# Optimization experiments

Hardware: AMD Instinct MI355X
Metric: run time of the kernel (lower is better)

## Reference

```python
import jax, jax.numpy as jnp
import numpy as np
from jax import lax

M, B, L, Q, S = 4, 64, 512, 512, 26  # models, batch, seq_len, hmm states, alphabet


def setup_inputs() -> dict:
    key = jax.random.key(0)
    k1, k2, k3, k4 = jax.random.split(key, 4)
    inputs = jax.random.uniform(k1, (M, B, L, S), dtype=jnp.float32)
    A_logits = jax.random.normal(k2, (M, Q, Q), dtype=jnp.float32)
    init_logits = jax.random.normal(k3, (M, Q), dtype=jnp.float32)
    em_logits = jax.random.normal(k4, (M, Q, S), dtype=jnp.float32)
    return {"inputs": inputs, "A_logits": A_logits,
            "init_logits": init_logits, "em_logits": em_logits}


def reference(inputs, A_logits, init_logits, em_logits):
    """Profile-HMM forward algorithm (scaled), as run by the MsaHmmCell RNN.

    inputs:      [M, B, L, S] observation probabilities (one-hot or soft)
    A_logits:    [M, Q, Q]    transition logits (row-softmax -> stochastic A)
    init_logits: [M, Q]       initial state distribution logits
    em_logits:   [M, Q, S]    emission logits (softmax over alphabet)
    returns loglik [M, B]  (the tensor the layer returns)
    """
    A = jax.nn.softmax(A_logits, axis=-1)        # [M, Q, Q]
    pi = jax.nn.softmax(init_logits, axis=-1)    # [M, Q]
    Bem = jax.nn.softmax(em_logits, axis=-1)     # [M, Q, S]

    # per-step emission likelihoods, time-major for scan: [L, M, B, Q]
    E = jnp.einsum('mbls,mqs->lmbq', inputs, Bem)

    # t = 0: alpha_0 = pi * e_0, scaled
    a0 = pi[:, None, :] * E[0]                   # [M, B, Q]
    s0 = jnp.sum(a0, axis=-1, keepdims=True)
    carry0 = (a0 / s0, jnp.log(s0[..., 0]))      # (alpha [M,B,Q], loglik [M,B])

    def step(carry, e_t):
        alpha, ll = carry
        r = jnp.einsum('mbq,mqp->mbp', alpha, A)  # transition
        a = r * e_t                               # emission
        s = jnp.sum(a, axis=-1, keepdims=True)    # scaling factor
        return (a / s, ll + jnp.log(s[..., 0])), None

    (alpha, loglik), _ = lax.scan(step, carry0, E[1:])
    return loglik  # [M, B] == reshape(loglik, (num_models, -1)) in the layer
```

## Files before the change

kernel.cpp:

```cpp
#include <hip/hip_runtime.h>
#include <hip/hip_bf16.h>
#include <math.h>


#define MM 4
#define BB 64
#define LL 512
#define QQ 512
#define SS 26
#define ASTR 528

typedef float f32x4 __attribute__((ext_vector_type(4)));
typedef int i32x4 __attribute__((ext_vector_type(4)));
typedef int i32x8 __attribute__((ext_vector_type(8)));

__device__ __forceinline__ float bf2f(unsigned short u) {
    return __uint_as_float(((unsigned)u) << 16);
}
__device__ __forceinline__ unsigned short f2bf(float f) {
    unsigned u = __float_as_uint(f);
    u = u + 0x7FFFu + ((u >> 16) & 1u);
    return (unsigned short)(u >> 16);
}
__device__ __forceinline__ unsigned char f2fp8(float x) {
    int r = __builtin_amdgcn_cvt_pk_fp8_f32(x, x, 0, false);
    return (unsigned char)(r & 0xFF);
}
__device__ __forceinline__ i32x8 ld32B(const unsigned char* p) {
    i32x4 lo = *(const i32x4*)p;
    i32x4 hi = *(const i32x4*)(p + 16);
    return __builtin_shufflevector(lo, hi, 0, 1, 2, 3, 4, 5, 6, 7);
}
__device__ __forceinline__ void barrier_lds() {
    __asm__ __volatile__("" ::: "memory");
    __builtin_amdgcn_s_waitcnt(0xC07F);
    __builtin_amdgcn_s_barrier();
    __asm__ __volatile__("" ::: "memory");
}


__global__ void prep_small(const float* __restrict__ il, const float* __restrict__ em,
                           float* __restrict__ pi, float* __restrict__ Bem) {
    int blk = blockIdx.x;
    int m = blk / (QQ + 1);
    int r = blk % (QQ + 1);
    int lane = threadIdx.x;
    if (r < QQ) {
        float x = (lane < SS) ? em[((size_t)m * QQ + r) * SS + lane] : -1e30f;
        float mx = x;
        #pragma unroll
        for (int o = 1; o < 64; o <<= 1) mx = fmaxf(mx, __shfl_xor(mx, o));
        float e = (lane < SS) ? __expf(x - mx) : 0.f;
        float s = e;
        #pragma unroll
        for (int o = 1; o < 64; o <<= 1) s += __shfl_xor(s, o);
        if (lane < SS) Bem[((size_t)m * QQ + r) * SS + lane] = e / s;
    } else {
        float v[8];
        float mx = -1e30f;
        #pragma unroll
        for (int k = 0; k < 8; ++k) { v[k] = il[m * QQ + k * 64 + lane]; mx = fmaxf(mx, v[k]); }
        #pragma unroll
        for (int o = 1; o < 64; o <<= 1) mx = fmaxf(mx, __shfl_xor(mx, o));
        float s = 0.f;
        #pragma unroll
        for (int k = 0; k < 8; ++k) { v[k] = __expf(v[k] - mx); s += v[k]; }
        #pragma unroll
        for (int o = 1; o < 64; o <<= 1) s += __shfl_xor(s, o);
        #pragma unroll
        for (int k = 0; k < 8; ++k) pi[m * QQ + k * 64 + lane] = v[k] / s;
    }
}

__global__ void prep_arow(const float* __restrict__ Al, float* __restrict__ Lrow) {
    int row = blockIdx.x;
    int lane = threadIdx.x;
    const float* p = Al + (size_t)row * QQ;
    float v[8];
    float mx = -1e30f;
    #pragma unroll
    for (int k = 0; k < 8; ++k) { v[k] = p[k * 64 + lane]; mx = fmaxf(mx, v[k]); }
    #pragma unroll
    for (int o = 1; o < 64; o <<= 1) mx = fmaxf(mx, __shfl_xor(mx, o));
    float s = 0.f;
    #pragma unroll
    for (int k = 0; k < 8; ++k) s += __expf(v[k] - mx);
    #pragma unroll
    for (int o = 1; o < 64; o <<= 1) s += __shfl_xor(s, o);
    if (lane == 0) Lrow[row] = mx + __logf(s);
}

__global__ void prep_atq(const float* __restrict__ Al, const float* __restrict__ Lrow,
                         unsigned char* __restrict__ Atq) {
    int bid = blockIdx.x;
    int m = bid >> 3, pb = bid & 7;
    __shared__ unsigned char tile[64][68];
    int l6 = threadIdx.x & 63, g = threadIdx.x >> 6;
    for (int c = 0; c < 8; ++c) {
        #pragma unroll
        for (int r = 0; r < 16; ++r) {
            int ql = g * 16 + r;
            int q = c * 64 + ql;
            float x = Al[((size_t)m * QQ + q) * QQ + pb * 64 + l6];
            tile[ql][l6] = f2fp8(__expf(x - Lrow[m * QQ + q]) * 256.f);
        }
        __syncthreads();
        #pragma unroll
        for (int r = 0; r < 16; ++r) {
            int pr = g * 16 + r;
            Atq[((size_t)m * QQ + pb * 64 + pr) * QQ + c * 64 + l6] = tile[l6][pr];
        }
        __syncthreads();
    }
}

__global__ void prep_e(const float* __restrict__ inp, const float* __restrict__ Bem,
                       unsigned short* __restrict__ E) {
    int bid = blockIdx.x;
    int tc = bid & 7;
    int b = (bid >> 3) & 63;
    int m = bid >> 9;
    int q0 = threadIdx.x;
    float bem0[SS], bem1[SS];
    const float* bp = Bem + (size_t)m * QQ * SS;
    #pragma unroll
    for (int j = 0; j < SS; ++j) bem0[j] = bp[(size_t)q0 * SS + j];
    #pragma unroll
    for (int j = 0; j < SS; ++j) bem1[j] = bp[(size_t)(q0 + 256) * SS + j];
    const float* ip = inp + (((size_t)(m * BB + b)) * LL + tc * 64) * SS;
    for (int lt = 0; lt < 64; ++lt) {
        int t = tc * 64 + lt;
        float a0 = 0.f, a1 = 0.f;
        #pragma unroll
        for (int j = 0; j < SS; ++j) {
            float x = ip[lt * SS + j];
            a0 += x * bem0[j];
            a1 += x * bem1[j];
        }
        size_t o = (((size_t)m * LL + t) * BB + b) * QQ + q0;
        E[o] = f2bf(a0);
        E[o + 256] = f2bf(a1);
    }
}


__launch_bounds__(512, 2)
__global__ void hmm_scan(const unsigned short* __restrict__ E,
                         const unsigned char* __restrict__ Atq,
                         const float* __restrict__ pi,
                         float* __restrict__ out) {
    const int c = blockIdx.x;
    const int m = c >> 2, bg = c & 3;
    const int tid = threadIdx.x;
    const int lane = tid & 63;
    const int wv = tid >> 6;
    const int sl = lane & 15;
    const int quad = lane >> 4;
    const float LOG256 = 5.545177444479562f;

    __shared__ unsigned char albuf[2][16 * ASTR];
    __shared__ __align__(16) float psl[2][16][20];
    __shared__ float Sfin[2][16];

    i32x8 breg[4][4];
    {
        const unsigned char* Ab = Atq + (size_t)m * QQ * QQ;
        #pragma unroll
        for (int h = 0; h < 4; ++h) {
            int p = wv * 64 + h * 16 + sl;
            const unsigned char* rp = Ab + (size_t)p * QQ + quad * 32;
            #pragma unroll
            for (int kc = 0; kc < 4; ++kc)
                breg[h][kc] = ld32B(rp + kc * 128);
        }
    }

    int wq[4];
    #pragma unroll
    for (int h = 0; h < 4; ++h)
        wq[h] = sl * ASTR + wv * 64 + h * 16 + quad * 4;

    const int b = bg * 16 + sl;
    const size_t ebase = (size_t)m * LL * BB * QQ;
    const ushort4* __restrict__ E4 = (const ushort4*)(E + ebase);
    const unsigned ESTR4 = (BB * QQ) >> 2;
    const unsigned ebq = (unsigned)(b * QQ) >> 2;
    unsigned eoffs[4];
    #pragma unroll
    for (int h = 0; h < 4; ++h) eoffs[h] = (unsigned)(wv * 16 + h * 4 + quad);

    float v[4][4];
    ushort4 ea[4], eb[4];

    float gcur, gprev, ll;

    {
        #pragma unroll
        for (int h = 0; h < 4; ++h) ea[h] = E4[ebq + ESTR4 + eoffs[h]];
        #pragma unroll
        for (int h = 0; h < 4; ++h) {
            int p0 = wv * 64 + h * 16 + quad * 4;
            f32x4 pv = *(const f32x4*)(pi + m * QQ + p0);
            ushort4 e0 = E4[ebq + eoffs[h]];
            v[h][0] = pv[0] * bf2f(e0.x);
            v[h][1] = pv[1] * bf2f(e0.y);
            v[h][2] = pv[2] * bf2f(e0.z);
            v[h][3] = pv[3] * bf2f(e0.w);
        }
        gcur = 256.f;
        gprev = 1.0f;
        unsigned char* ab = &albuf[0][0];
        #pragma unroll
        for (int h = 0; h < 4; ++h) {
            int d = __builtin_amdgcn_cvt_pk_fp8_f32(gcur * v[h][0], gcur * v[h][1], 0, false);
            d = __builtin_amdgcn_cvt_pk_fp8_f32(gcur * v[h][2], gcur * v[h][3], d, true);
            *(int*)(ab + wq[h]) = d;
        }
        float ps = ((v[0][0] + v[0][1]) + (v[0][2] + v[0][3]))
                 + ((v[1][0] + v[1][1]) + (v[1][2] + v[1][3]))
                 + ((v[2][0] + v[2][1]) + (v[2][2] + v[2][3]))
                 + ((v[3][0] + v[3][1]) + (v[3][2] + v[3][3]));
        ps += __shfl_xor(ps, 16);
        if ((quad & 1) == 0) psl[0][sl][2 * wv + (quad >> 1)] = ps;
        ll = -(__logf(gcur) + LOG256);
        barrier_lds();
    }

    auto body = [&](int par, bool first, ushort4 (&ecur)[4], ushort4 (&enxt)[4],
                    unsigned epre) {
        #pragma unroll
        for (int h = 0; h < 4; ++h) enxt[h] = E4[epre + eoffs[h]];

        if (wv == 0 && lane < 16) {
            const f32x4* pr = (const f32x4*)&psl[par][lane][0];
            f32x4 ss4 = (pr[0] + pr[1]) + (pr[2] + pr[3]);
            Sfin[par][lane] = (ss4[0] + ss4[1]) + (ss4[2] + ss4[3]);
        }
        float lam = first ? 16384.0f
                          : 16384.0f * gcur * gprev * Sfin[par ^ 1][sl];
        float gnext = 128.0f * __builtin_amdgcn_rcpf(lam);

        const unsigned char* ar = &albuf[par][0] + sl * ASTR + quad * 32;
        i32x8 af0 = ld32B(ar);
        i32x8 af1 = ld32B(ar + 128);
        i32x8 af2 = ld32B(ar + 256);
        i32x8 af3 = ld32B(ar + 384);

        unsigned char* ab = &albuf[par ^ 1][0];
        float ps = 0.f;
        #pragma unroll
        for (int h = 0; h < 4; ++h) {
            f32x4 acc = (f32x4){0.f, 0.f, 0.f, 0.f};
            acc = __builtin_amdgcn_mfma_scale_f32_16x16x128_f8f6f4(
                breg[h][0], af0, acc, 0, 0, 0, 0x7F7F7F7F, 0, 0x7F7F7F7F);
            acc = __builtin_amdgcn_mfma_scale_f32_16x16x128_f8f6f4(
                breg[h][1], af1, acc, 0, 0, 0, 0x7F7F7F7F, 0, 0x7F7F7F7F);
            acc = __builtin_amdgcn_mfma_scale_f32_16x16x128_f8f6f4(
                breg[h][2], af2, acc, 0, 0, 0, 0x7F7F7F7F, 0, 0x7F7F7F7F);
            acc = __builtin_amdgcn_mfma_scale_f32_16x16x128_f8f6f4(
                breg[h][3], af3, acc, 0, 0, 0, 0x7F7F7F7F, 0, 0x7F7F7F7F);
            v[h][0] = acc[0] * bf2f(ecur[h].x);
            v[h][1] = acc[1] * bf2f(ecur[h].y);
            v[h][2] = acc[2] * bf2f(ecur[h].z);
            v[h][3] = acc[3] * bf2f(ecur[h].w);
            int d = __builtin_amdgcn_cvt_pk_fp8_f32(gnext * v[h][0], gnext * v[h][1], 0, false);
            d = __builtin_amdgcn_cvt_pk_fp8_f32(gnext * v[h][2], gnext * v[h][3], d, true);
            *(int*)(ab + wq[h]) = d;
            ps += (v[h][0] + v[h][1]) + (v[h][2] + v[h][3]);
        }
        ps += __shfl_xor(ps, 16);
        if ((quad & 1) == 0) psl[par ^ 1][sl][2 * wv + (quad >> 1)] = ps;
        ll -= __logf(gnext) + LOG256;
        gprev = gcur; gcur = gnext;
        barrier_lds();
    };

    unsigned epre = ebq + 2 * ESTR4;
    body(0, true,  ea, eb, epre); epre += ESTR4;
    body(1, false, eb, ea, epre); epre += ESTR4;
    for (int t = 2; t < LL - 2; t += 2) {
        body(0, false, ea, eb, epre); epre += ESTR4;
        body(1, false, eb, ea, epre); epre += ESTR4;
    }
    {
        const unsigned char* ar = &albuf[0][0] + sl * ASTR + quad * 32;
        i32x8 af0 = ld32B(ar);
        i32x8 af1 = ld32B(ar + 128);
        i32x8 af2 = ld32B(ar + 256);
        i32x8 af3 = ld32B(ar + 384);
        #pragma unroll
        for (int h = 0; h < 4; ++h) {
            f32x4 acc = (f32x4){0.f, 0.f, 0.f, 0.f};
            acc = __builtin_amdgcn_mfma_scale_f32_16x16x128_f8f6f4(
                breg[h][0], af0, acc, 0, 0, 0, 0x7F7F7F7F, 0, 0x7F7F7F7F);
            acc = __builtin_amdgcn_mfma_scale_f32_16x16x128_f8f6f4(
                breg[h][1], af1, acc, 0, 0, 0, 0x7F7F7F7F, 0, 0x7F7F7F7F);
            acc = __builtin_amdgcn_mfma_scale_f32_16x16x128_f8f6f4(
                breg[h][2], af2, acc, 0, 0, 0, 0x7F7F7F7F, 0, 0x7F7F7F7F);
            acc = __builtin_amdgcn_mfma_scale_f32_16x16x128_f8f6f4(
                breg[h][3], af3, acc, 0, 0, 0, 0x7F7F7F7F, 0, 0x7F7F7F7F);
            v[h][0] = acc[0] * bf2f(ea[h].x);
            v[h][1] = acc[1] * bf2f(ea[h].y);
            v[h][2] = acc[2] * bf2f(ea[h].z);
            v[h][3] = acc[3] * bf2f(ea[h].w);
        }
    }

    {
        float ps = ((v[0][0] + v[0][1]) + (v[0][2] + v[0][3]))
                 + ((v[1][0] + v[1][1]) + (v[1][2] + v[1][3]))
                 + ((v[2][0] + v[2][1]) + (v[2][2] + v[2][3]))
                 + ((v[3][0] + v[3][1]) + (v[3][2] + v[3][3]));
        ps += __shfl_xor(ps, 16);
        if ((quad & 1) == 0) psl[1][sl][2 * wv + (quad >> 1)] = ps;
        __syncthreads();
        if (wv == 0 && lane < 16) {
            const f32x4* pr = (const f32x4*)&psl[1][lane][0];
            f32x4 ss4 = (pr[0] + pr[1]) + (pr[2] + pr[3]);
            float S = (ss4[0] + ss4[1]) + (ss4[2] + ss4[3]);
            out[m * BB + bg * 16 + lane] = ll + __logf(S);
        }
    }
}


extern "C" void kernel_launch(void* const* d_in, const int* in_sizes, int n_in,
                              void* d_out, int out_size, void* d_ws, size_t ws_size,
                              hipStream_t stream) {
    const float* inputs = (const float*)d_in[0];
    const float* A_logits = (const float*)d_in[1];
    const float* init_logits = (const float*)d_in[2];
    const float* em_logits = (const float*)d_in[3];
    float* out = (float*)d_out;

    char* ws = (char*)d_ws;
    size_t off = 0;
    unsigned short* E = (unsigned short*)(ws + off);  off += (size_t)MM * LL * BB * QQ * 2;
    unsigned char* Atq = (unsigned char*)(ws + off);  off += (size_t)MM * QQ * QQ;
    float* Bem = (float*)(ws + off);                  off += (size_t)MM * QQ * SS * 4;
    float* pi = (float*)(ws + off);                   off += (size_t)MM * QQ * 4;
    float* Lrow = (float*)(ws + off);                 off += (size_t)MM * QQ * 4;

    if (ws_size < off) {
        (void)hipMemsetAsync(d_out, 0, (size_t)out_size * sizeof(float), stream);
        return;
    }

    prep_small<<<dim3(MM * (QQ + 1)), dim3(64), 0, stream>>>(init_logits, em_logits, pi, Bem);
    prep_arow<<<dim3(MM * QQ), dim3(64), 0, stream>>>(A_logits, Lrow);
    prep_atq<<<dim3(MM * 8), dim3(256), 0, stream>>>(A_logits, Lrow, Atq);
    prep_e<<<dim3(MM * BB * 8), dim3(256), 0, stream>>>(inputs, Bem, E);
    hmm_scan<<<dim3(16), dim3(512), 0, stream>>>(E, Atq, pi, out);
}
```

Baseline: 619.6 us.

## Triple-buffer partial sums and split MFMA chains to shorten per-step critical path

Every thread now reduces the previous step's partial sums itself from a triple-buffered psl array. This replaces the old scheme where wave 0 wrote Sfin and the other threads read it one step later, and removes that extra dependency stage. The MFMA K-reduction is split into two independent accumulator chains, interleaved across the four output tiles, and summed at the end, so the dependent MFMA latency chain per tile is shorter. The cost is more redundant LDS reads for the reduction and more accumulator registers.

```diff
diff --git a/kernel.cpp b/kernel.cpp
--- a/kernel.cpp
+++ b/kernel.cpp
@@ -31,6 +31,8 @@
     i32x4 hi = *(const i32x4*)(p + 16);
     return __builtin_shufflevector(lo, hi, 0, 1, 2, 3, 4, 5, 6, 7);
 }
+#define MFMA8(A, B, C) __builtin_amdgcn_mfma_scale_f32_16x16x128_f8f6f4( \
+    (A), (B), (C), 0, 0, 0, 0x7F7F7F7F, 0, 0x7F7F7F7F)
 __device__ __forceinline__ void barrier_lds() {
     __asm__ __volatile__("" ::: "memory");
     __builtin_amdgcn_s_waitcnt(0xC07F);
@@ -159,8 +161,7 @@
     const float LOG256 = 5.545177444479562f;
 
     __shared__ unsigned char albuf[2][16 * ASTR];
-    __shared__ __align__(16) float psl[2][16][20];
-    __shared__ float Sfin[2][16];
+    __shared__ __align__(16) float psl[3][16][20];
 
     i32x8 breg[4][4];
     {
@@ -226,84 +227,141 @@
         barrier_lds();
     }
 
-    auto body = [&](int par, bool first, ushort4 (&ecur)[4], ushort4 (&enxt)[4],
-                    unsigned epre) {
+    auto body = [&](int par, bool first, int rs, int ws,
+                    ushort4 (&ecur)[4], ushort4 (&enxt)[4], unsigned epre) {
         #pragma unroll
         for (int h = 0; h < 4; ++h) enxt[h] = E4[epre + eoffs[h]];
 
-        if (wv == 0 && lane < 16) {
-            const f32x4* pr = (const f32x4*)&psl[par][lane][0];
+        float lam;
+        if (first) {
+            lam = 16384.0f;
+        } else {
+            const f32x4* pr = (const f32x4*)&psl[rs][sl][0];
             f32x4 ss4 = (pr[0] + pr[1]) + (pr[2] + pr[3]);
-            Sfin[par][lane] = (ss4[0] + ss4[1]) + (ss4[2] + ss4[3]);
-        }
-        float lam = first ? 16384.0f
-                          : 16384.0f * gcur * gprev * Sfin[par ^ 1][sl];
+            float Sp = (ss4[0] + ss4[1]) + (ss4[2] + ss4[3]);
+            lam = 16384.0f * gcur * gprev * Sp;
+        }
         float gnext = 128.0f * __builtin_amdgcn_rcpf(lam);
 
         const unsigned char* ar = &albuf[par][0] + sl * ASTR + quad * 32;
         i32x8 af0 = ld32B(ar);
+        i32x8 af2 = ld32B(ar + 256);
         i32x8 af1 = ld32B(ar + 128);
-        i32x8 af2 = ld32B(ar + 256);
         i32x8 af3 = ld32B(ar + 384);
 
+        f32x4 z = (f32x4){0.f, 0.f, 0.f, 0.f};
+        f32x4 aA0, aA1, aA2, aA3, aB0, aB1, aB2, aB3;
+        aA0 = MFMA8(breg[0][0], af0, z);
+        aA1 = MFMA8(breg[1][0], af0, z);
+        aA2 = MFMA8(breg[2][0], af0, z);
+        aA3 = MFMA8(breg[3][0], af0, z);
+        aB0 = MFMA8(breg[0][2], af2, z);
+        aB1 = MFMA8(breg[1][2], af2, z);
+        aB2 = MFMA8(breg[2][2], af2, z);
+        aB3 = MFMA8(breg[3][2], af2, z);
+        aA0 = MFMA8(breg[0][1], af1, aA0);
+        aA1 = MFMA8(breg[1][1], af1, aA1);
+        aA2 = MFMA8(breg[2][1], af1, aA2);
+        aA3 = MFMA8(breg[3][1], af1, aA3);
+        aB0 = MFMA8(breg[0][3], af3, aB0);
+        aB1 = MFMA8(breg[1][3], af3, aB1);
+        aB2 = MFMA8(breg[2][3], af3, aB2);
+        aB3 = MFMA8(breg[3][3], af3, aB3);
+
+        f32x4 t0 = aA0 + aB0;
+        f32x4 t1 = aA1 + aB1;
+        f32x4 t2 = aA2 + aB2;
+        f32x4 t3 = aA3 + aB3;
         unsigned char* ab = &albuf[par ^ 1][0];
-        float ps = 0.f;
+        v[0][0] = t0[0] * bf2f(ecur[0].x);
+        v[0][1] = t0[1] * bf2f(ecur[0].y);
+        v[0][2] = t0[2] * bf2f(ecur[0].z);
+        v[0][3] = t0[3] * bf2f(ecur[0].w);
+        v[1][0] = t1[0] * bf2f(ecur[1].x);
+        v[1][1] = t1[1] * bf2f(ecur[1].y);
+        v[1][2] = t1[2] * bf2f(ecur[1].z);
+        v[1][3] = t1[3] * bf2f(ecur[1].w);
+        v[2][0] = t2[0] * bf2f(ecur[2].x);
+        v[2][1] = t2[1] * bf2f(ecur[2].y);
+        v[2][2] = t2[2] * bf2f(ecur[2].z);
+        v[2][3] = t2[3] * bf2f(ecur[2].w);
+        v[3][0] = t3[0] * bf2f(ecur[3].x);
+        v[3][1] = t3[1] * bf2f(ecur[3].y);
+        v[3][2] = t3[2] * bf2f(ecur[3].z);
+        v[3][3] = t3[3] * bf2f(ecur[3].w);
         #pragma unroll
         for (int h = 0; h < 4; ++h) {
-            f32x4 acc = (f32x4){0.f, 0.f, 0.f, 0.f};
-            acc = __builtin_amdgcn_mfma_scale_f32_16x16x128_f8f6f4(
-                breg[h][0], af0, acc, 0, 0, 0, 0x7F7F7F7F, 0, 0x7F7F7F7F);
-            acc = __builtin_amdgcn_mfma_scale_f32_16x16x128_f8f6f4(
-                breg[h][1], af1, acc, 0, 0, 0, 0x7F7F7F7F, 0, 0x7F7F7F7F);
-            acc = __builtin_amdgcn_mfma_scale_f32_16x16x128_f8f6f4(
-                breg[h][2], af2, acc, 0, 0, 0, 0x7F7F7F7F, 0, 0x7F7F7F7F);
-            acc = __builtin_amdgcn_mfma_scale_f32_16x16x128_f8f6f4(
-                breg[h][3], af3, acc, 0, 0, 0, 0x7F7F7F7F, 0, 0x7F7F7F7F);
-            v[h][0] = acc[0] * bf2f(ecur[h].x);
-            v[h][1] = acc[1] * bf2f(ecur[h].y);
-            v[h][2] = acc[2] * bf2f(ecur[h].z);
-            v[h][3] = acc[3] * bf2f(ecur[h].w);
             int d = __builtin_amdgcn_cvt_pk_fp8_f32(gnext * v[h][0], gnext * v[h][1], 0, false);
             d = __builtin_amdgcn_cvt_pk_fp8_f32(gnext * v[h][2], gnext * v[h][3], d, true);
             *(int*)(ab + wq[h]) = d;
-            ps += (v[h][0] + v[h][1]) + (v[h][2] + v[h][3]);
-        }
+        }
+        float ps = ((v[0][0] + v[0][1]) + (v[0][2] + v[0][3]))
+                 + ((v[1][0] + v[1][1]) + (v[1][2] + v[1][3]))
+                 + ((v[2][0] + v[2][1]) + (v[2][2] + v[2][3]))
+                 + ((v[3][0] + v[3][1]) + (v[3][2] + v[3][3]));
         ps += __shfl_xor(ps, 16);
-        if ((quad & 1) == 0) psl[par ^ 1][sl][2 * wv + (quad >> 1)] = ps;
+        if ((quad & 1) == 0) psl[ws][sl][2 * wv + (quad >> 1)] = ps;
         ll -= __logf(gnext) + LOG256;
         gprev = gcur; gcur = gnext;
         barrier_lds();
     };
 
     unsigned epre = ebq + 2 * ESTR4;
-    body(0, true,  ea, eb, epre); epre += ESTR4;
-    body(1, false, eb, ea, epre); epre += ESTR4;
-    for (int t = 2; t < LL - 2; t += 2) {
-        body(0, false, ea, eb, epre); epre += ESTR4;
-        body(1, false, eb, ea, epre); epre += ESTR4;
+    body(0, true,  2, 1, ea, eb, epre); epre += ESTR4;
+    body(1, false, 0, 2, eb, ea, epre); epre += ESTR4;
+    {
+        int rs = 1, ws = 0;
+        for (int t = 2; t < LL - 2; t += 2) {
+            body(0, false, rs, ws, ea, eb, epre); epre += ESTR4;
+            rs = (rs == 2) ? 0 : rs + 1; ws = (ws == 2) ? 0 : ws + 1;
+            body(1, false, rs, ws, eb, ea, epre); epre += ESTR4;
+            rs = (rs == 2) ? 0 : rs + 1; ws = (ws == 2) ? 0 : ws + 1;
+        }
     }
     {
         const unsigned char* ar = &albuf[0][0] + sl * ASTR + quad * 32;
         i32x8 af0 = ld32B(ar);
+        i32x8 af2 = ld32B(ar + 256);
         i32x8 af1 = ld32B(ar + 128);
-        i32x8 af2 = ld32B(ar + 256);
         i32x8 af3 = ld32B(ar + 384);
-        #pragma unroll
-        for (int h = 0; h < 4; ++h) {
-            f32x4 acc = (f32x4){0.f, 0.f, 0.f, 0.f};
-            acc = __builtin_amdgcn_mfma_scale_f32_16x16x128_f8f6f4(
-                breg[h][0], af0, acc, 0, 0, 0, 0x7F7F7F7F, 0, 0x7F7F7F7F);
-            acc = __builtin_amdgcn_mfma_scale_f32_16x16x128_f8f6f4(
-                breg[h][1], af1, acc, 0, 0, 0, 0x7F7F7F7F, 0, 0x7F7F7F7F);
-            acc = __builtin_amdgcn_mfma_scale_f32_16x16x128_f8f6f4(
-                breg[h][2], af2, acc, 0, 0, 0, 0x7F7F7F7F, 0, 0x7F7F7F7F);
-            acc = __builtin_amdgcn_mfma_scale_f32_16x16x128_f8f6f4(
-                breg[h][3], af3, acc, 0, 0, 0, 0x7F7F7F7F, 0, 0x7F7F7F7F);
-            v[h][0] = acc[0] * bf2f(ea[h].x);
-            v[h][1] = acc[1] * bf2f(ea[h].y);
-            v[h][2] = acc[2] * bf2f(ea[h].z);
-            v[h][3] = acc[3] * bf2f(ea[h].w);
-        }
+        f32x4 z = (f32x4){0.f, 0.f, 0.f, 0.f};
+        f32x4 aA0, aA1, aA2, aA3, aB0, aB1, aB2, aB3;
+        aA0 = MFMA8(breg[0][0], af0, z);
+        aA1 = MFMA8(breg[1][0], af0, z);
+        aA2 = MFMA8(breg[2][0], af0, z);
+        aA3 = MFMA8(breg[3][0], af0, z);
+        aB0 = MFMA8(breg[0][2], af2, z);
+        aB1 = MFMA8(breg[1][2], af2, z);
+        aB2 = MFMA8(breg[2][2], af2, z);
+        aB3 = MFMA8(breg[3][2], af2, z);
+        aA0 = MFMA8(breg[0][1], af1, aA0);
+        aA1 = MFMA8(breg[1][1], af1, aA1);
+        aA2 = MFMA8(breg[2][1], af1, aA2);
+        aA3 = MFMA8(breg[3][1], af1, aA3);
+        aB0 = MFMA8(breg[0][3], af3, aB0);
+        aB1 = MFMA8(breg[1][3], af3, aB1);
+        aB2 = MFMA8(breg[2][3], af3, aB2);
+        aB3 = MFMA8(breg[3][3], af3, aB3);
+        f32x4 t0 = aA0 + aB0;
+        f32x4 t1 = aA1 + aB1;
+        f32x4 t2 = aA2 + aB2;
+        f32x4 t3 = aA3 + aB3;
+        v[0][0] = t0[0] * bf2f(ea[0].x);
+        v[0][1] = t0[1] * bf2f(ea[0].y);
+        v[0][2] = t0[2] * bf2f(ea[0].z);
+        v[0][3] = t0[3] * bf2f(ea[0].w);
+        v[1][0] = t1[0] * bf2f(ea[1].x);
+        v[1][1] = t1[1] * bf2f(ea[1].y);
+        v[1][2] = t1[2] * bf2f(ea[1].z);
+        v[1][3] = t1[3] * bf2f(ea[1].w);
+        v[2][0] = t2[0] * bf2f(ea[2].x);
+        v[2][1] = t2[1] * bf2f(ea[2].y);
+        v[2][2] = t2[2] * bf2f(ea[2].z);
+        v[2][3] = t2[3] * bf2f(ea[2].w);
+        v[3][0] = t3[0] * bf2f(ea[3].x);
+        v[3][1] = t3[1] * bf2f(ea[3].y);
+        v[3][2] = t3[2] * bf2f(ea[3].z);
+        v[3][3] = t3[3] * bf2f(ea[3].w);
     }
 
     {
```

Result: slower. 668.1 us (+7.8%).
